# Kernel tuning notes

Hardware: AMD Instinct MI355X
Metric: run time of the kernel (lower is better)

Reference implementation:

```python
import jax, jax.numpy as jnp
import numpy as np

B, C, H, W = 8, 256, 64, 64
D = C // 8  # qk proj dim = 32
R = C // 8  # channel-SE reduction dim = 32

def setup_inputs() -> dict:
    key = jax.random.key(0)
    ks = jax.random.split(key, 10)
    s = lambda *sh: 1.0 / np.sqrt(sh[-1])
    return {
        'x':  jax.random.normal(ks[0], (B, C, H, W), jnp.float32),
        'Wq': jax.random.normal(ks[1], (D, C), jnp.float32) * s(D, C),
        'bq': jnp.zeros((D,), jnp.float32),
        'Wk': jax.random.normal(ks[2], (D, C), jnp.float32) * s(D, C),
        'bk': jnp.zeros((D,), jnp.float32),
        'Wv': jax.random.normal(ks[3], (C, C), jnp.float32) * s(C, C),
        'bv': jnp.zeros((C,), jnp.float32),
        'gamma': jnp.ones((1,), jnp.float32),
        'W1': jax.random.normal(ks[4], (R, 2 * C), jnp.float32) * s(R, 2 * C),
        'W2': jax.random.normal(ks[5], (C, R), jnp.float32) * s(C, R),
        'lamb': jnp.ones((1,), jnp.float32),
    }

def reference(x, Wq, bq, Wk, bk, Wv, bv, gamma, W1, W2, lamb):
    b, c, h, w = x.shape
    n = h * w
    xf = x.reshape(b, c, n)  # [B,C,N]
    # --- spatial self-attention (1x1 convs == matmuls over channel dim) ---
    q = jnp.einsum('dc,bcn->bnd', Wq, xf) + bq            # [B,N,D]
    k = jnp.einsum('dc,bcn->bdn', Wk, xf) + bk[:, None]   # [B,D,N]
    attn = jax.nn.softmax(jnp.einsum('bnd,bdm->bnm', q, k), axis=-1)  # [B,N,N]
    v = jnp.einsum('dc,bcn->bdn', Wv, xf) + bv[:, None]   # [B,C,N]
    # out[b,c,m] = sum_n v[b,c,n] * attn[b,m,n]  (torch: bmm(v, attn^T))
    sp = jnp.einsum('bcn,bmn->bcm', v, attn).reshape(b, c, h, w)
    sp = gamma * sp
    # --- channel SE-gate ---
    mean = jnp.mean(xf, axis=-1)                # [B,C]
    std = jnp.std(xf, axis=-1, ddof=1)          # torch.std uses unbiased (ddof=1)
    inp = jnp.concatenate([mean, std], axis=1)  # [B,2C]
    a = jax.nn.sigmoid(jax.nn.relu(inp @ W1.T) @ W2.T)  # [B,C]
    ch = lamb * a[:, :, None, None] * x
    return sp + ch + x
```

## Files before the change

### kernel.cpp

```cpp
#include <hip/hip_runtime.h>
#include <hip/hip_bf16.h>

#define Bb 8
#define Cc 256
#define Nn 4096
#define Dd 32

typedef short bf16x8 __attribute__((ext_vector_type(8)));
typedef short bf16x4 __attribute__((ext_vector_type(4)));
typedef float f32x4 __attribute__((ext_vector_type(4)));

__device__ __forceinline__ void glds16(const void* g, void* l) {
    __builtin_amdgcn_global_load_lds(
        (const __attribute__((address_space(1))) unsigned int*)g,
        (__attribute__((address_space(3))) unsigned int*)l, 16, 0, 0);
}

__global__ __launch_bounds__(256) void convt_kernel(
    const float* __restrict__ x, __hip_bfloat16* __restrict__ x_t,
    float* __restrict__ sum_ws, float* __restrict__ sumsq_ws)
{
    __shared__ __hip_bfloat16 tile[64][68];
    const int n0 = blockIdx.x * 64, c0 = blockIdx.y * 64, b = blockIdx.z;
    const int t = threadIdx.x;

#pragma unroll
    for (int i = 0; i < 4; i++) {
        int id = i * 256 + t;
        int row = id >> 4, col4 = id & 15;
        float4 v = *(const float4*)(x + ((size_t)(b * Cc + c0 + row)) * Nn + n0 + col4 * 4);
        bf16x4 bv;
        bv[0] = __bfloat16_as_short(__float2bfloat16(v.x));
        bv[1] = __bfloat16_as_short(__float2bfloat16(v.y));
        bv[2] = __bfloat16_as_short(__float2bfloat16(v.z));
        bv[3] = __bfloat16_as_short(__float2bfloat16(v.w));
        *(bf16x4*)((void*)&tile[row][col4 * 4]) = bv;
        float ls  = v.x + v.y + v.z + v.w;
        float ls2 = v.x * v.x + v.y * v.y + v.z * v.z + v.w * v.w;
        ls  += __shfl_xor(ls, 1, 16);  ls2 += __shfl_xor(ls2, 1, 16);
        ls  += __shfl_xor(ls, 2, 16);  ls2 += __shfl_xor(ls2, 2, 16);
        ls  += __shfl_xor(ls, 4, 16);  ls2 += __shfl_xor(ls2, 4, 16);
        ls  += __shfl_xor(ls, 8, 16);  ls2 += __shfl_xor(ls2, 8, 16);
        if ((t & 15) == 0) {
            atomicAdd(&sum_ws[b * Cc + c0 + row], ls);
            atomicAdd(&sumsq_ws[b * Cc + c0 + row], ls2);
        }
    }
    __syncthreads();
#pragma unroll
    for (int i = 0; i < 2; i++) {
        int id = i * 256 + t;
        int nl = id >> 3, cg = id & 7;
        bf16x8 o;
#pragma unroll
        for (int j = 0; j < 8; j++) o[j] = __bfloat16_as_short(tile[cg * 8 + j][nl]);
        *(bf16x8*)(x_t + ((size_t)(b * Nn + n0 + nl)) * Cc + c0 + cg * 8) = o;
    }
}

__global__ __launch_bounds__(256) void wconv_kernel(
    const float* __restrict__ Wq, const float* __restrict__ Wk, const float* __restrict__ Wv,
    __hip_bfloat16* __restrict__ w_bf)
{
    const int ct = blockIdx.x;
    const int t = threadIdx.x;
#pragma unroll
    for (int i = 0; i < 8; i++) {
        int g = i * 256 + t;
        int row = g >> 5, c8 = g & 31;
        int c0 = c8 * 8;
        int grow = ct * 64 + row;
        const float* src;
        if (grow < 32)       src = Wq + (size_t)grow * Cc + c0;
        else if (grow < 64)  src = Wk + (size_t)(grow - 32) * Cc + c0;
        else                 src = Wv + (size_t)(grow - 64) * Cc + c0;
        float4 v0 = *(const float4*)src;
        float4 v1 = *(const float4*)(src + 4);
        bf16x8 o;
        o[0] = __bfloat16_as_short(__float2bfloat16(v0.x));
        o[1] = __bfloat16_as_short(__float2bfloat16(v0.y));
        o[2] = __bfloat16_as_short(__float2bfloat16(v0.z));
        o[3] = __bfloat16_as_short(__float2bfloat16(v0.w));
        o[4] = __bfloat16_as_short(__float2bfloat16(v1.x));
        o[5] = __bfloat16_as_short(__float2bfloat16(v1.y));
        o[6] = __bfloat16_as_short(__float2bfloat16(v1.z));
        o[7] = __bfloat16_as_short(__float2bfloat16(v1.w));
        int kchunk = c0 >> 5, qd = (c0 & 31) >> 3, cg = row >> 4, rl = row & 15;
        *(bf16x8*)(w_bf + ((size_t)ct * 32 + kchunk * 4 + cg) * 512 + (qd * 16 + rl) * 8) = o;
    }
}

__global__ __launch_bounds__(256, 2) void proj_kernel(
    const __hip_bfloat16* __restrict__ x_t, const __hip_bfloat16* __restrict__ w_bf,
    const float* __restrict__ bq, const float* __restrict__ bk, const float* __restrict__ bv,
    __hip_bfloat16* __restrict__ q_ws, __hip_bfloat16* __restrict__ k_ws,
    __hip_bfloat16* __restrict__ v_ws)
{
    __shared__ __hip_bfloat16 ldsX[32 * 512];
    __shared__ __hip_bfloat16 ldsW[32 * 512];

    const int n0 = blockIdx.x * 64;
    const int ct = blockIdx.y;
    const int b  = blockIdx.z;
    const int t = threadIdx.x;
    const int w = t >> 6, lane = t & 63, quad = lane >> 4, l15 = lane & 15;

#pragma unroll
    for (int j = 0; j < 8; j++) {
        int idx = w * 8 + j;
        int kchunk = idx >> 2, ngrp = idx & 3;
        glds16(x_t + ((size_t)(b * Nn + n0 + ngrp * 16 + l15)) * Cc + kchunk * 32 + quad * 8,
               ldsX + idx * 512);
        glds16(w_bf + ((size_t)ct * 32 + idx) * 512 + lane * 8, ldsW + idx * 512);
    }
    __syncthreads();

    f32x4 acc[4];
#pragma unroll
    for (int cg = 0; cg < 4; cg++) {
        int gcol = ct * 64 + cg * 16 + l15;
        float bias = (gcol < 32) ? bq[gcol] : (gcol < 64 ? bk[gcol - 32] : bv[gcol - 64]);
        acc[cg] = (f32x4){bias, bias, bias, bias};
    }

#pragma unroll
    for (int kchunk = 0; kchunk < 8; kchunk++) {
        bf16x8 a = *(const bf16x8*)(ldsX + ((kchunk * 4 + w) * 64 + lane) * 8);
#pragma unroll
        for (int cg = 0; cg < 4; cg++) {
            bf16x8 bw = *(const bf16x8*)(ldsW + ((kchunk * 4 + cg) * 64 + lane) * 8);
            acc[cg] = __builtin_amdgcn_mfma_f32_16x16x32_bf16(a, bw, acc[cg], 0, 0, 0);
        }
    }

#pragma unroll
    for (int cg = 0; cg < 4; cg++) {
        int gcol = ct * 64 + cg * 16 + l15;
        int nb = n0 + w * 16 + quad * 4;
        if (gcol < 64) {
            __hip_bfloat16* dst = (gcol < 32) ? q_ws : k_ws;
            int d = gcol & 31;
#pragma unroll
            for (int r = 0; r < 4; r++)
                dst[((size_t)(b * Nn + nb + r)) * Dd + d] = __float2bfloat16(acc[cg][r]);
        } else {
            int c = gcol - 64;
            bf16x4 o;
#pragma unroll
            for (int r = 0; r < 4; r++) o[r] = __bfloat16_as_short(__float2bfloat16(acc[cg][r]));
            *(bf16x4*)(v_ws + ((size_t)(b * Cc + c)) * Nn + nb) = o;
        }
    }
}

__global__ __launch_bounds__(256) void gate_kernel(
    const float* __restrict__ sum_ws, const float* __restrict__ sumsq_ws,
    const float* __restrict__ W1, const float* __restrict__ W2,
    const float* __restrict__ lamb, float* __restrict__ coef)
{
    int b = blockIdx.x;
    __shared__ float inp[2 * Cc];
    __shared__ float h[32];
    int t = threadIdx.x;
    float s  = sum_ws[b * Cc + t];
    float s2 = sumsq_ws[b * Cc + t];
    float m   = s / Nn;
    float var = (s2 - (float)Nn * m * m) / (float)(Nn - 1);
    inp[t]      = m;
    inp[Cc + t] = sqrtf(fmaxf(var, 0.f));
    __syncthreads();
    if (t < 32) {
        float a = 0.f;
        for (int i = 0; i < 2 * Cc; i++) a += W1[t * (2 * Cc) + i] * inp[i];
        h[t] = fmaxf(a, 0.f);
    }
    __syncthreads();
    float g = 0.f;
#pragma unroll
    for (int r = 0; r < 32; r++) g += W2[t * 32 + r] * h[r];
    float a = 1.f / (1.f + __expf(-g));
    coef[b * Cc + t] = 1.f + lamb[0] * a;
}

__global__ __launch_bounds__(512, 2) void attn_kernel(
    const __hip_bfloat16* __restrict__ q_ws, const __hip_bfloat16* __restrict__ k_ws,
    const __hip_bfloat16* __restrict__ v_ws, const float* __restrict__ coef,
    const float* __restrict__ x, const float* __restrict__ gamma_p,
    float* __restrict__ out)
{
    extern __shared__ __hip_bfloat16 smem[];
    __hip_bfloat16* vbuf0 = smem;
    __hip_bfloat16* vbuf1 = smem + 16384;
    __hip_bfloat16* kbuf0 = smem + 32768;
    __hip_bfloat16* kbuf1 = smem + 36864;
    __hip_bfloat16* pbuf0 = smem + 40960;
    __hip_bfloat16* pbuf1 = smem + 49152;

    const int b  = blockIdx.x & 7;
    const int m0 = (blockIdx.x >> 3) * 128;
    const int t = threadIdx.x;
    const int w = t >> 6, lane = t & 63, quad = lane >> 4, l15 = lane & 15;
    const int mf0 = (w >> 1) * 2, chalf = w & 1;

    const bf16x8 aq = *(const bf16x8*)(q_ws + ((size_t)(b * Nn + m0 + w * 16 + l15)) * Dd + quad * 8);

    const __hip_bfloat16* vsrc[4];
#pragma unroll
    for (int j = 0; j < 4; j++) {
        int idx = w * 4 + j;
        int ch = idx >> 4, tc = idx & 15;
        vsrc[j] = v_ws + ((size_t)(b * Cc + tc * 16 + l15)) * Nn + ch * 32 + quad * 8;
    }
    const __hip_bfloat16* ksrc = k_ws + ((size_t)(b * Nn + w * 16 + l15)) * Dd + quad * 8;

#pragma unroll
    for (int j = 0; j < 4; j++) glds16(vsrc[j], vbuf0 + (w * 4 + j) * 512);
    glds16(ksrc, kbuf0 + w * 512);
    __syncthreads();

    f32x4 acc[2][8];
#pragma unroll
    for (int i = 0; i < 2; i++)
#pragma unroll
        for (int j = 0; j < 8; j++) acc[i][j] = (f32x4){0.f, 0.f, 0.f, 0.f};
    f32x4 accl[2] = {(f32x4){0.f,0.f,0.f,0.f}, (f32x4){0.f,0.f,0.f,0.f}};

    bf16x8 ones;
#pragma unroll
    for (int i = 0; i < 8; i++) ones[i] = (short)0x3F80;

    for (int it = 0; it < Nn / 64; it++) {
        const __hip_bfloat16* kb = (((it >> 1) & 1) ? kbuf1 : kbuf0) + (it & 1) * 2048;
        f32x4 s[4];
#pragma unroll
        for (int tt = 0; tt < 4; tt++) {
            bf16x8 bk = *(const bf16x8*)(kb + (tt * 64 + lane) * 8);
            s[tt] = __builtin_amdgcn_mfma_f32_16x16x32_bf16(aq, bk, (f32x4){0.f,0.f,0.f,0.f}, 0, 0, 0);
        }
        __hip_bfloat16* pb = (it & 1) ? pbuf1 : pbuf0;
#pragma unroll
        for (int tt = 0; tt < 4; tt++) {
            int nn = (tt & 1) * 16 + l15;
            __hip_bfloat16* pd = pb + (w * 2 + (tt >> 1)) * 512
                               + ((nn >> 3) * 16 + quad * 4) * 8 + (nn & 7);
#pragma unroll
            for (int r = 0; r < 4; r++)
                pd[r * 8] = __float2bfloat16(__expf(s[tt][r]));
        }

        __syncthreads();

        if (it + 1 < Nn / 64) {
            __hip_bfloat16* vn = ((it + 1) & 1) ? vbuf1 : vbuf0;
#pragma unroll
            for (int j = 0; j < 4; j++)
                glds16(vsrc[j] + (size_t)(it + 1) * 64, vn + (w * 4 + j) * 512);
        }
        if ((it & 1) == 0 && it + 2 < Nn / 64) {
            int sl = (it >> 1) + 1;
            glds16(ksrc + (size_t)(sl * 128) * Dd, ((sl & 1) ? kbuf1 : kbuf0) + w * 512);
        }

        const __hip_bfloat16* vb = (it & 1) ? vbuf1 : vbuf0;
        const __hip_bfloat16* pr = pb;
#pragma unroll
        for (int kc = 0; kc < 2; kc++) {
            bf16x8 ap0 = *(const bf16x8*)(pr + (((mf0    ) * 2 + kc) * 64 + lane) * 8);
            bf16x8 ap1 = *(const bf16x8*)(pr + (((mf0 + 1) * 2 + kc) * 64 + lane) * 8);
            accl[0] = __builtin_amdgcn_mfma_f32_16x16x32_bf16(ap0, ones, accl[0], 0, 0, 0);
            accl[1] = __builtin_amdgcn_mfma_f32_16x16x32_bf16(ap1, ones, accl[1], 0, 0, 0);
#pragma unroll
            for (int tcl = 0; tcl < 8; tcl++) {
                bf16x8 bv = *(const bf16x8*)(vb + ((kc * 16 + chalf * 8 + tcl) * 64 + lane) * 8);
                acc[0][tcl] = __builtin_amdgcn_mfma_f32_16x16x32_bf16(ap0, bv, acc[0][tcl], 0, 0, 0);
                acc[1][tcl] = __builtin_amdgcn_mfma_f32_16x16x32_bf16(ap1, bv, acc[1][tcl], 0, 0, 0);
            }
        }
    }

    const float g = gamma_p[0];
    float inv[2][4];
#pragma unroll
    for (int mfi = 0; mfi < 2; mfi++)
#pragma unroll
        for (int r = 0; r < 4; r++) inv[mfi][r] = g / accl[mfi][r];

#pragma unroll
    for (int mfi = 0; mfi < 2; mfi++) {
#pragma unroll
        for (int tcl = 0; tcl < 8; tcl++) {
            int c = (chalf * 8 + tcl) * 16 + l15;
            float cf = coef[b * Cc + c];
            size_t base = ((size_t)(b * Cc + c)) * Nn + m0 + (mf0 + mfi) * 16 + quad * 4;
#pragma unroll
            for (int r = 0; r < 4; r++)
                out[base + r] = acc[mfi][tcl][r] * inv[mfi][r] + cf * x[base + r];
        }
    }
}

extern "C" void kernel_launch(void* const* d_in, const int* in_sizes, int n_in,
                              void* d_out, int out_size, void* d_ws, size_t ws_size,
                              hipStream_t stream) {
    const float* x     = (const float*)d_in[0];
    const float* Wq    = (const float*)d_in[1];
    const float* bq    = (const float*)d_in[2];
    const float* Wk    = (const float*)d_in[3];
    const float* bk    = (const float*)d_in[4];
    const float* Wv    = (const float*)d_in[5];
    const float* bv    = (const float*)d_in[6];
    const float* gamma = (const float*)d_in[7];
    const float* W1    = (const float*)d_in[8];
    const float* W2    = (const float*)d_in[9];
    const float* lamb  = (const float*)d_in[10];
    float* out = (float*)d_out;

    char* ws = (char*)d_ws;
    __hip_bfloat16* q_ws = (__hip_bfloat16*)ws;
    __hip_bfloat16* k_ws = (__hip_bfloat16*)(ws + (2u  << 20));
    __hip_bfloat16* v_ws = (__hip_bfloat16*)(ws + (4u  << 20));
    __hip_bfloat16* x_t  = (__hip_bfloat16*)(ws + (20u << 20));
    float* sum_ws   = (float*)(ws + (36u << 20));
    float* sumsq_ws = sum_ws + Bb * Cc;
    float* coef     = sumsq_ws + Bb * Cc;
    __hip_bfloat16* w_bf = (__hip_bfloat16*)(ws + (37u << 20));

    (void)hipFuncSetAttribute((const void*)attn_kernel,
                              hipFuncAttributeMaxDynamicSharedMemorySize, 114688);

    hipMemsetAsync(sum_ws, 0, 2 * Bb * Cc * sizeof(float), stream);
    wconv_kernel<<<5, 256, 0, stream>>>(Wq, Wk, Wv, w_bf);
    convt_kernel<<<dim3(Nn / 64, Cc / 64, Bb), 256, 0, stream>>>(x, x_t, sum_ws, sumsq_ws);
    proj_kernel<<<dim3(Nn / 64, 5, Bb), 256, 0, stream>>>(x_t, w_bf, bq, bk, bv, q_ws, k_ws, v_ws);
    gate_kernel<<<Bb, 256, 0, stream>>>(sum_ws, sumsq_ws, W1, W2, lamb, coef);
    attn_kernel<<<256, 512, 114688, stream>>>(q_ws, k_ws, v_ws, coef, x, gamma, out);
}
```

Baseline: 248.4 us.

## Keep attention probabilities in registers via transposed QK^T and permlane swaps

Computes S^T = K·Q per wave so each wave produces the probabilities for its own query rows. The exp'd scores are packed to bf16 and rearranged with permlane32_swap into the MFMA B operand, so the LDS round-trip for P goes away. A permuted K row order (sl15) lines the layout up. Row sums are now accumulated in scalar registers with cross-lane shuffles instead of an MFMA against a ones vector. LDS drops from 112KB to 80KB and the sync moves to the end of the iteration, but each wave now does 2x the QK MFMAs and exps, since QK work is duplicated across the chalf wave pairs.

```diff
diff --git a/kernel.cpp b/kernel.cpp
--- a/kernel.cpp
+++ b/kernel.cpp
@@ -9,11 +9,17 @@
 typedef short bf16x8 __attribute__((ext_vector_type(8)));
 typedef short bf16x4 __attribute__((ext_vector_type(4)));
 typedef float f32x4 __attribute__((ext_vector_type(4)));
+typedef unsigned int u32;
 
 __device__ __forceinline__ void glds16(const void* g, void* l) {
     __builtin_amdgcn_global_load_lds(
         (const __attribute__((address_space(1))) unsigned int*)g,
         (__attribute__((address_space(3))) unsigned int*)l, 16, 0, 0);
+}
+
+__device__ __forceinline__ u32 pkbf16(float a, float b) {
+    return ((u32)__bfloat16_as_ushort(__float2bfloat16(b)) << 16) |
+           (u32)__bfloat16_as_ushort(__float2bfloat16(a));
 }
 
 __global__ __launch_bounds__(256) void convt_kernel(
@@ -193,16 +199,15 @@
     __hip_bfloat16* vbuf1 = smem + 16384;
     __hip_bfloat16* kbuf0 = smem + 32768;
     __hip_bfloat16* kbuf1 = smem + 36864;
-    __hip_bfloat16* pbuf0 = smem + 40960;
-    __hip_bfloat16* pbuf1 = smem + 49152;
 
     const int b  = blockIdx.x & 7;
     const int m0 = (blockIdx.x >> 3) * 128;
     const int t = threadIdx.x;
     const int w = t >> 6, lane = t & 63, quad = lane >> 4, l15 = lane & 15;
-    const int mf0 = (w >> 1) * 2, chalf = w & 1;
-
-    const bf16x8 aq = *(const bf16x8*)(q_ws + ((size_t)(b * Nn + m0 + w * 16 + l15)) * Dd + quad * 8);
+    const int chalf = w & 1, mf0 = (w >> 1) * 2;
+
+    const bf16x8 aq0 = *(const bf16x8*)(q_ws + ((size_t)(b * Nn + m0 + (mf0 + 0) * 16 + l15)) * Dd + quad * 8);
+    const bf16x8 aq1 = *(const bf16x8*)(q_ws + ((size_t)(b * Nn + m0 + (mf0 + 1) * 16 + l15)) * Dd + quad * 8);
 
     const __hip_bfloat16* vsrc[4];
 #pragma unroll
@@ -211,7 +216,8 @@
         int ch = idx >> 4, tc = idx & 15;
         vsrc[j] = v_ws + ((size_t)(b * Cc + tc * 16 + l15)) * Nn + ch * 32 + quad * 8;
     }
-    const __hip_bfloat16* ksrc = k_ws + ((size_t)(b * Nn + w * 16 + l15)) * Dd + quad * 8;
+    const int sl15 = (l15 & 3) | ((l15 & 4) << 1) | ((l15 & 8) >> 1);
+    const __hip_bfloat16* ksrc = k_ws + ((size_t)(b * Nn + w * 16 + sl15)) * Dd + quad * 8;
 
 #pragma unroll
     for (int j = 0; j < 4; j++) glds16(vsrc[j], vbuf0 + (w * 4 + j) * 512);
@@ -223,33 +229,9 @@
     for (int i = 0; i < 2; i++)
 #pragma unroll
         for (int j = 0; j < 8; j++) acc[i][j] = (f32x4){0.f, 0.f, 0.f, 0.f};
-    f32x4 accl[2] = {(f32x4){0.f,0.f,0.f,0.f}, (f32x4){0.f,0.f,0.f,0.f}};
-
-    bf16x8 ones;
-#pragma unroll
-    for (int i = 0; i < 8; i++) ones[i] = (short)0x3F80;
+    float lsum0 = 0.f, lsum1 = 0.f;
 
     for (int it = 0; it < Nn / 64; it++) {
-        const __hip_bfloat16* kb = (((it >> 1) & 1) ? kbuf1 : kbuf0) + (it & 1) * 2048;
-        f32x4 s[4];
-#pragma unroll
-        for (int tt = 0; tt < 4; tt++) {
-            bf16x8 bk = *(const bf16x8*)(kb + (tt * 64 + lane) * 8);
-            s[tt] = __builtin_amdgcn_mfma_f32_16x16x32_bf16(aq, bk, (f32x4){0.f,0.f,0.f,0.f}, 0, 0, 0);
-        }
-        __hip_bfloat16* pb = (it & 1) ? pbuf1 : pbuf0;
-#pragma unroll
-        for (int tt = 0; tt < 4; tt++) {
-            int nn = (tt & 1) * 16 + l15;
-            __hip_bfloat16* pd = pb + (w * 2 + (tt >> 1)) * 512
-                               + ((nn >> 3) * 16 + quad * 4) * 8 + (nn & 7);
-#pragma unroll
-            for (int r = 0; r < 4; r++)
-                pd[r * 8] = __float2bfloat16(__expf(s[tt][r]));
-        }
-
-        __syncthreads();
-
         if (it + 1 < Nn / 64) {
             __hip_bfloat16* vn = ((it + 1) & 1) ? vbuf1 : vbuf0;
 #pragma unroll
@@ -261,40 +243,57 @@
             glds16(ksrc + (size_t)(sl * 128) * Dd, ((sl & 1) ? kbuf1 : kbuf0) + w * 512);
         }
 
+        const __hip_bfloat16* kb = (((it >> 1) & 1) ? kbuf1 : kbuf0) + (it & 1) * 2048;
+        u32 pk0[4][2], pk1[4][2];
+#pragma unroll
+        for (int tt = 0; tt < 4; tt++) {
+            bf16x8 ak = *(const bf16x8*)(kb + (tt * 64 + lane) * 8);
+            f32x4 s0 = __builtin_amdgcn_mfma_f32_16x16x32_bf16(ak, aq0, (f32x4){0.f,0.f,0.f,0.f}, 0, 0, 0);
+            f32x4 s1 = __builtin_amdgcn_mfma_f32_16x16x32_bf16(ak, aq1, (f32x4){0.f,0.f,0.f,0.f}, 0, 0, 0);
+            float a0 = __expf(s0[0]), a1 = __expf(s0[1]), a2 = __expf(s0[2]), a3 = __expf(s0[3]);
+            lsum0 += (a0 + a1) + (a2 + a3);
+            pk0[tt][0] = pkbf16(a0, a1);
+            pk0[tt][1] = pkbf16(a2, a3);
+            float b0 = __expf(s1[0]), b1 = __expf(s1[1]), b2 = __expf(s1[2]), b3 = __expf(s1[3]);
+            lsum1 += (b0 + b1) + (b2 + b3);
+            pk1[tt][0] = pkbf16(b0, b1);
+            pk1[tt][1] = pkbf16(b2, b3);
+        }
+
         const __hip_bfloat16* vb = (it & 1) ? vbuf1 : vbuf0;
-        const __hip_bfloat16* pr = pb;
-#pragma unroll
-        for (int kc = 0; kc < 2; kc++) {
-            bf16x8 ap0 = *(const bf16x8*)(pr + (((mf0    ) * 2 + kc) * 64 + lane) * 8);
-            bf16x8 ap1 = *(const bf16x8*)(pr + (((mf0 + 1) * 2 + kc) * 64 + lane) * 8);
-            accl[0] = __builtin_amdgcn_mfma_f32_16x16x32_bf16(ap0, ones, accl[0], 0, 0, 0);
-            accl[1] = __builtin_amdgcn_mfma_f32_16x16x32_bf16(ap1, ones, accl[1], 0, 0, 0);
-#pragma unroll
-            for (int tcl = 0; tcl < 8; tcl++) {
-                bf16x8 bv = *(const bf16x8*)(vb + ((kc * 16 + chalf * 8 + tcl) * 64 + lane) * 8);
-                acc[0][tcl] = __builtin_amdgcn_mfma_f32_16x16x32_bf16(ap0, bv, acc[0][tcl], 0, 0, 0);
-                acc[1][tcl] = __builtin_amdgcn_mfma_f32_16x16x32_bf16(ap1, bv, acc[1][tcl], 0, 0, 0);
+#pragma unroll
+        for (int nc = 0; nc < 2; nc++) {
+            auto g0 = __builtin_amdgcn_permlane32_swap(pk0[2 * nc][0], pk0[2 * nc + 1][0], false, false);
+            auto g1 = __builtin_amdgcn_permlane32_swap(pk0[2 * nc][1], pk0[2 * nc + 1][1], false, false);
+            auto h0 = __builtin_amdgcn_permlane32_swap(pk1[2 * nc][0], pk1[2 * nc + 1][0], false, false);
+            auto h1 = __builtin_amdgcn_permlane32_swap(pk1[2 * nc][1], pk1[2 * nc + 1][1], false, false);
+            union { u32 uw[4]; bf16x8 v; } bp0, bp1;
+            bp0.uw[0] = g0[0]; bp0.uw[1] = g1[0]; bp0.uw[2] = g0[1]; bp0.uw[3] = g1[1];
+            bp1.uw[0] = h0[0]; bp1.uw[1] = h1[0]; bp1.uw[2] = h0[1]; bp1.uw[3] = h1[1];
+#pragma unroll
+            for (int cf = 0; cf < 8; cf++) {
+                bf16x8 av = *(const bf16x8*)(vb + (((nc * 16) + chalf * 8 + cf) * 64 + lane) * 8);
+                acc[0][cf] = __builtin_amdgcn_mfma_f32_16x16x32_bf16(av, bp0.v, acc[0][cf], 0, 0, 0);
+                acc[1][cf] = __builtin_amdgcn_mfma_f32_16x16x32_bf16(av, bp1.v, acc[1][cf], 0, 0, 0);
             }
         }
-    }
-
+        __syncthreads();
+    }
+
+    lsum0 += __shfl_xor(lsum0, 16); lsum0 += __shfl_xor(lsum0, 32);
+    lsum1 += __shfl_xor(lsum1, 16); lsum1 += __shfl_xor(lsum1, 32);
     const float g = gamma_p[0];
-    float inv[2][4];
-#pragma unroll
-    for (int mfi = 0; mfi < 2; mfi++)
-#pragma unroll
-        for (int r = 0; r < 4; r++) inv[mfi][r] = g / accl[mfi][r];
-
-#pragma unroll
-    for (int mfi = 0; mfi < 2; mfi++) {
-#pragma unroll
-        for (int tcl = 0; tcl < 8; tcl++) {
-            int c = (chalf * 8 + tcl) * 16 + l15;
-            float cf = coef[b * Cc + c];
-            size_t base = ((size_t)(b * Cc + c)) * Nn + m0 + (mf0 + mfi) * 16 + quad * 4;
-#pragma unroll
-            for (int r = 0; r < 4; r++)
-                out[base + r] = acc[mfi][tcl][r] * inv[mfi][r] + cf * x[base + r];
+    const float inv0 = g / lsum0, inv1 = g / lsum1;
+
+#pragma unroll
+    for (int cf = 0; cf < 8; cf++) {
+#pragma unroll
+        for (int r = 0; r < 4; r++) {
+            int c = chalf * 128 + cf * 16 + quad * 4 + r;
+            float cfv = coef[b * Cc + c];
+            size_t base = ((size_t)(b * Cc + c)) * Nn + m0 + mf0 * 16 + l15;
+            out[base]      = acc[0][cf][r] * inv0 + cfv * x[base];
+            out[base + 16] = acc[1][cf][r] * inv1 + cfv * x[base + 16];
         }
     }
 }
@@ -326,12 +325,12 @@
     __hip_bfloat16* w_bf = (__hip_bfloat16*)(ws + (37u << 20));
 
     (void)hipFuncSetAttribute((const void*)attn_kernel,
-                              hipFuncAttributeMaxDynamicSharedMemorySize, 114688);
+                              hipFuncAttributeMaxDynamicSharedMemorySize, 81920);
 
     hipMemsetAsync(sum_ws, 0, 2 * Bb * Cc * sizeof(float), stream);
     wconv_kernel<<<5, 256, 0, stream>>>(Wq, Wk, Wv, w_bf);
     convt_kernel<<<dim3(Nn / 64, Cc / 64, Bb), 256, 0, stream>>>(x, x_t, sum_ws, sumsq_ws);
     proj_kernel<<<dim3(Nn / 64, 5, Bb), 256, 0, stream>>>(x_t, w_bf, bq, bk, bv, q_ws, k_ws, v_ws);
     gate_kernel<<<Bb, 256, 0, stream>>>(sum_ws, sumsq_ws, W1, W2, lamb, coef);
-    attn_kernel<<<256, 512, 114688, stream>>>(q_ws, k_ws, v_ws, coef, x, gamma, out);
-}
+    attn_kernel<<<256, 512, 81920, stream>>>(q_ws, k_ws, v_ws, coef, x, gamma, out);
+}
```

Result: slower. 260.3 us (+4.8%).
